# Optimization experiments

Hardware: AMD Instinct MI355X
Metric: run time of the kernel (lower is better)

## Reference

```python
import jax, jax.numpy as jnp
import numpy as np

B, T, E, H = 4, 1024, 1024, 16
D = E // H  # head_size = 64
EPS = 1e-5


def layernorm(x, g, b):
    mu = jnp.mean(x, axis=-1, keepdims=True)
    var = jnp.mean(jnp.square(x - mu), axis=-1, keepdims=True)
    return (x - mu) * jax.lax.rsqrt(var + EPS) * g + b


def setup_inputs() -> dict:
    key = jax.random.key(0)
    ks = jax.random.split(key, 12)
    s = 0.02
    return {
        "x": jax.random.normal(ks[0], (B, T, E), dtype=jnp.float32),
        "ln1_g": jnp.ones((E,), jnp.float32),
        "ln1_b": jnp.zeros((E,), jnp.float32),
        "Wq": jax.random.normal(ks[1], (H, E, D), dtype=jnp.float32) * s,
        "Wk": jax.random.normal(ks[2], (H, E, D), dtype=jnp.float32) * s,
        "Wv": jax.random.normal(ks[3], (H, E, D), dtype=jnp.float32) * s,
        "Wp": jax.random.normal(ks[4], (E, E), dtype=jnp.float32) * s,
        "bp": jnp.zeros((E,), jnp.float32),
        "ln2_g": jnp.ones((E,), jnp.float32),
        "ln2_b": jnp.zeros((E,), jnp.float32),
        "W1": jax.random.normal(ks[5], (E, 4 * E), dtype=jnp.float32) * s,
        "b1": jnp.zeros((4 * E,), jnp.float32),
        "W2": jax.random.normal(ks[6], (4 * E, E), dtype=jnp.float32) * s,
        "b2": jnp.zeros((E,), jnp.float32),
    }


def reference(x, ln1_g, ln1_b, Wq, Wk, Wv, Wp, bp, ln2_g, ln2_b, W1, b1, W2, b2):
    # --- attention sub-block (pre-LN) ---
    h = layernorm(x, ln1_g, ln1_b)               # [B,T,E]
    q = jnp.einsum('bte,hed->bhtd', h, Wq)       # [B,H,T,D]
    k = jnp.einsum('bte,hed->bhtd', h, Wk)
    v = jnp.einsum('bte,hed->bhtd', h, Wv)
    # NOTE: original module has NO 1/sqrt(D) scaling and its 'tril' buffer is
    # all-ones, so masked_fill is a no-op -> full (non-causal) softmax.
    scores = jnp.einsum('bhtd,bhsd->bhts', q, k)  # [B,H,T,T]
    attn = jax.nn.softmax(scores, axis=-1)
    o = jnp.einsum('bhts,bhsd->bhtd', attn, v)    # [B,H,T,D]
    o = o.transpose(0, 2, 1, 3).reshape(x.shape[0], x.shape[1], -1)  # [B,T,E]
    x = x + o @ Wp + bp
    # --- feedforward sub-block (dropout is identity at eval) ---
    h2 = layernorm(x, ln2_g, ln2_b)
    x = x + jax.nn.relu(h2 @ W1 + b1) @ W2 + b2
    return x
```

## Files before the change

### kernel.cpp

```cpp
#include <hip/hip_runtime.h>
#include <hip/hip_bf16.h>

#define BB 4
#define TT 1024
#define EE 1024
#define HH 16
#define DD 64
#define MM 4096
#define NQKV 3072
#define E4 4096

using short8  = __attribute__((ext_vector_type(8))) short;
using short4v = __attribute__((ext_vector_type(4))) short;
using f32x4   = __attribute__((ext_vector_type(4))) float;

__device__ __forceinline__ short f2bf(float f) {
    __hip_bfloat16 h = __float2bfloat16(f);
    return *reinterpret_cast<short*>(&h);
}

__device__ __forceinline__ unsigned int cvtpk_bf16(float a, float b) {
    unsigned int w;
    asm("v_cvt_pk_bf16_f32 %0, %1, %2" : "=v"(w) : "v"(a), "v"(b));
    return w;
}

__device__ __forceinline__ void gld16(const void* g, void* l) {
    __builtin_amdgcn_global_load_lds((__attribute__((address_space(1))) void*)g,
                                     (__attribute__((address_space(3))) void*)l,
                                     16, 0, 0);
}

__global__ __launch_bounds__(256) void tcvt_kernel(const float* __restrict__ in,
                                                   short* __restrict__ out,
                                                   int R, int C) {
    __shared__ short tile[64][65];
    const int c0 = blockIdx.x * 64, r0 = blockIdx.y * 64;
    const int tr = threadIdx.x >> 6;
    const int tc = threadIdx.x & 63;
#pragma unroll
    for (int i = 0; i < 16; ++i) {
        int r = i * 4 + tr;
        tile[tc][r] = f2bf(in[(size_t)(r0 + r) * C + c0 + tc]);
    }
    __syncthreads();
#pragma unroll
    for (int i = 0; i < 16; ++i) {
        int c = i * 4 + tr;
        out[(size_t)(c0 + c) * R + r0 + tc] = tile[c][tc];
    }
}

__global__ __launch_bounds__(256) void pack_qkv_t(const float* __restrict__ Wq,
                                                  const float* __restrict__ Wk,
                                                  const float* __restrict__ Wv,
                                                  short* __restrict__ out) {
    __shared__ short tile[64][65];
    const int m = blockIdx.y;
    const int which = m >> 4, head = m & 15;
    const float* src = ((which == 0) ? Wq : (which == 1) ? Wk : Wv) + (size_t)head * EE * DD;
    const float scale = (which == 1) ? 1.44269504f : 1.0f;
    const int e0 = blockIdx.x * 64;
    const int tr = threadIdx.x >> 6, tc = threadIdx.x & 63;
#pragma unroll
    for (int i = 0; i < 16; ++i) {
        int e = i * 4 + tr;
        tile[tc][e] = f2bf(src[(size_t)(e0 + e) * DD + tc] * scale);
    }
    __syncthreads();
#pragma unroll
    for (int i = 0; i < 16; ++i) {
        int d = i * 4 + tr;
        out[(size_t)(which * 1024 + head * 64 + d) * EE + e0 + tc] = tile[d][tc];
    }
}

__global__ __launch_bounds__(256) void vtr_kernel(const short* __restrict__ qkv,
                                                  short* __restrict__ vT) {
    __shared__ short tile[64][68];
    const int b = blockIdx.z;
    const int t0 = blockIdx.x * 64, c0 = blockIdx.y * 64;
    const int tr = threadIdx.x >> 4;
    const int q4 = (threadIdx.x & 15) * 4;
#pragma unroll
    for (int i = 0; i < 4; ++i) {
        int t = i * 16 + tr;
        short4v v = *(const short4v*)&qkv[((size_t)b * TT + t0 + t) * NQKV + 2048 + c0 + q4];
        *(short4v*)&tile[t][q4] = v;
    }
    __syncthreads();
#pragma unroll
    for (int i = 0; i < 4; ++i) {
        int c = i * 16 + tr;
        short4v v;
        v[0] = tile[q4 + 0][c];
        v[1] = tile[q4 + 1][c];
        v[2] = tile[q4 + 2][c];
        v[3] = tile[q4 + 3][c];
        *(short4v*)&vT[((size_t)b * 1024 + c0 + c) * TT + t0 + q4] = v;
    }
}

__global__ __launch_bounds__(256) void ln_kernel(const float* __restrict__ x,
                                                 const float* __restrict__ g,
                                                 const float* __restrict__ b,
                                                 short* __restrict__ out) {
    __shared__ float red[4];
    const int row = blockIdx.x;
    const int tid = threadIdx.x;
    float4 v = *(const float4*)&x[(size_t)row * EE + tid * 4];
    float s = v.x + v.y + v.z + v.w;
#pragma unroll
    for (int off = 32; off >= 1; off >>= 1) s += __shfl_xor(s, off, 64);
    if ((tid & 63) == 0) red[tid >> 6] = s;
    __syncthreads();
    float mean = (red[0] + red[1] + red[2] + red[3]) * (1.0f / EE);
    __syncthreads();
    float d0 = v.x - mean, d1 = v.y - mean, d2 = v.z - mean, d3 = v.w - mean;
    s = d0 * d0 + d1 * d1 + d2 * d2 + d3 * d3;
#pragma unroll
    for (int off = 32; off >= 1; off >>= 1) s += __shfl_xor(s, off, 64);
    if ((tid & 63) == 0) red[tid >> 6] = s;
    __syncthreads();
    float var = (red[0] + red[1] + red[2] + red[3]) * (1.0f / EE);
    float rstd = rsqrtf(var + 1e-5f);
    int c = tid * 4;
    short4v o;
    o[0] = f2bf(d0 * rstd * g[c + 0] + b[c + 0]);
    o[1] = f2bf(d1 * rstd * g[c + 1] + b[c + 1]);
    o[2] = f2bf(d2 * rstd * g[c + 2] + b[c + 2]);
    o[3] = f2bf(d3 * rstd * g[c + 3] + b[c + 3]);
    *(short4v*)&out[(size_t)row * EE + c] = o;
}

template <int BN, int PIPE, bool HAS_BIAS, bool RELU, bool RESID, bool OUT_BF16>
__global__ __launch_bounds__(256) void gemm_bt(const short* __restrict__ A,
                                               const short* __restrict__ Bt,
                                               const float* __restrict__ bias,
                                               const float* __restrict__ resid,
                                               void* __restrict__ outp,
                                               int M, int N, int K) {
    constexpr int WRC = (BN == 128) ? 2 : 4;
    constexpr int WCC = (BN == 128) ? 2 : 1;
    constexpr int MI = 8 / WRC;
    constexpr int NI = BN / (16 * WCC);
    constexpr int BCH = BN / 32;
    constexpr int ASZ = 128 * 64, BSZ = BN * 64;

    __shared__ __align__(16) short As[(PIPE ? 2 : 1) * ASZ];
    __shared__ __align__(16) short Bs[(PIPE ? 2 : 1) * BSZ];

    const int tid = threadIdx.x;
    const int lane = tid & 63;
    const int wid = tid >> 6;
    const int wr = (WRC == 2) ? (wid >> 1) : wid;
    const int wc = (WCC == 2) ? (wid & 1) : 0;
    const int l15 = lane & 15, lhi = lane >> 4;

    int wg = blockIdx.y * gridDim.x + blockIdx.x;
    const int chunk = (gridDim.x * gridDim.y) >> 3;
    wg = (wg & 7) * chunk + (wg >> 3);
    const int bx = wg % gridDim.x;
    const int by = wg / gridDim.x;
    const int row0 = by * 128, col0 = bx * BN;

    const int srow = tid >> 3;
    const int scol = (((tid & 7) ^ (srow & 7)) << 3);
    const int rsw = l15 & 7;

    const int wrow0 = wr * (16 * MI);
    const int wcol0 = wc * (16 * NI);

    f32x4 acc[MI][NI] = {};

    auto stage = [&](int k0, int bs) {
#pragma unroll
        for (int ch = 0; ch < 4; ++ch)
            gld16(&A[(size_t)(row0 + ch * 32 + srow) * K + k0 + scol],
                  &As[bs * ASZ + ch * 2048 + wid * 512]);
#pragma unroll
        for (int ch = 0; ch < BCH; ++ch)
            gld16(&Bt[(size_t)(col0 + ch * 32 + srow) * K + k0 + scol],
                  &Bs[bs * BSZ + ch * 2048 + wid * 512]);
    };
    auto compute = [&](int bs) {
#pragma unroll
        for (int ks = 0; ks < 2; ++ks) {
            short8 af[MI], bf[NI];
#pragma unroll
            for (int mi = 0; mi < MI; ++mi)
                af[mi] = *(const short8*)&As[bs * ASZ + (wrow0 + mi * 16 + l15) * 64 +
                                             (((ks << 2) + lhi) ^ rsw) * 8];
#pragma unroll
            for (int ni = 0; ni < NI; ++ni)
                bf[ni] = *(const short8*)&Bs[bs * BSZ + (wcol0 + ni * 16 + l15) * 64 +
                                             (((ks << 2) + lhi) ^ rsw) * 8];
#pragma unroll
            for (int mi = 0; mi < MI; ++mi)
#pragma unroll
                for (int ni = 0; ni < NI; ++ni)
                    acc[mi][ni] = __builtin_amdgcn_mfma_f32_16x16x32_bf16(
                        af[mi], bf[ni], acc[mi][ni], 0, 0, 0);
        }
    };

    if (PIPE == 1) {
        const int nt = K >> 6;
        stage(0, 0);
        stage(64, 1);
        int cur = 0;
        for (int t = 0; t < nt; ++t) {
            if (t + 1 < nt) asm volatile("s_waitcnt vmcnt(6)" ::: "memory");
            else            asm volatile("s_waitcnt vmcnt(0)" ::: "memory");
            __builtin_amdgcn_s_barrier();
            __builtin_amdgcn_sched_barrier(0);
            compute(cur);
            __builtin_amdgcn_sched_barrier(0);
            __builtin_amdgcn_s_barrier();
            if (t + 2 < nt) stage((t + 2) << 6, cur);
            cur ^= 1;
        }
    } else {
        for (int k0 = 0; k0 < K; k0 += 64) {
            __syncthreads();
            stage(k0, 0);
            __syncthreads();
            compute(0);
        }
    }

    float* outf = (float*)outp;
    short* outb = (short*)outp;
#pragma unroll
    for (int mi = 0; mi < MI; ++mi)
#pragma unroll
        for (int ni = 0; ni < NI; ++ni)
#pragma unroll
            for (int r = 0; r < 4; ++r) {
                int row = row0 + wrow0 + mi * 16 + lhi * 4 + r;
                int col = col0 + wcol0 + ni * 16 + l15;
                float v = acc[mi][ni][r];
                if (HAS_BIAS) v += bias[col];
                if (RELU) v = fmaxf(v, 0.f);
                if (RESID) v += resid[(size_t)row * N + col];
                if (OUT_BF16) outb[(size_t)row * N + col] = f2bf(v);
                else outf[(size_t)row * N + col] = v;
            }
}

__global__ __launch_bounds__(256) void attn_kernel(const short* __restrict__ qkv,
                                                   const short* __restrict__ vT,
                                                   short* __restrict__ obuf) {
    __shared__ __align__(16) short Ks[2][64 * 64];
    __shared__ __align__(16) short Vs[2][64 * 64];
    __shared__ __align__(16) unsigned int Pl[4][2][16][40];
    const int tid = threadIdx.x;
    const int lane = tid & 63;
    const int wid = tid >> 6;
    const int l15 = lane & 15, lhi = lane >> 4;
    const int lhi4 = lhi * 4;

    const int nb = ((blockIdx.x & 7) << 6) + (blockIdx.x >> 3);
    const int b = nb >> 7;
    const int h = (nb >> 3) & 15;
    const int q0 = (nb & 7) << 7;
    const size_t rbase = (size_t)b * TT;
    const int hq = h * 64;
    const short* vg = vT + ((size_t)b * 1024 + hq) * TT;

    const int srow = tid >> 3;
    const int scol = (((tid & 7) ^ (srow & 7)) << 3);
    const int rsw = (l15 & 7);

    short8 aq[2][2];
#pragma unroll
    for (int g = 0; g < 2; ++g)
#pragma unroll
        for (int ks = 0; ks < 2; ++ks)
            aq[g][ks] = *(const short8*)&qkv[(rbase + q0 + wid * 32 + g * 16 + l15) * NQKV +
                                             hq + ks * 32 + lhi * 8];

    float mrun[2] = {-INFINITY, -INFINITY};
    float lsum[2] = {0.f, 0.f};
    f32x4 o[2][4] = {};

#pragma unroll
    for (int ch = 0; ch < 2; ++ch) {
        gld16(&qkv[(rbase + 0 + ch * 32 + srow) * NQKV + 1024 + hq + scol],
              &Ks[0][ch * 2048 + wid * 512]);
        gld16(&vg[(size_t)(ch * 32 + srow) * TT + 0 + scol],
              &Vs[0][ch * 2048 + wid * 512]);
    }
    __syncthreads();

    int cur = 0;
    for (int st = 0; st < TT; st += 64) {
        if (st + 64 < TT) {
#pragma unroll
            for (int ch = 0; ch < 2; ++ch) {
                gld16(&qkv[(rbase + st + 64 + ch * 32 + srow) * NQKV + 1024 + hq + scol],
                      &Ks[cur ^ 1][ch * 2048 + wid * 512]);
                gld16(&vg[(size_t)(ch * 32 + srow) * TT + st + 64 + scol],
                      &Vs[cur ^ 1][ch * 2048 + wid * 512]);
            }
        }
        const short* K = &Ks[cur][0];
        const short* V = &Vs[cur][0];

        short8 kf[4][2];
#pragma unroll
        for (int nt = 0; nt < 4; ++nt)
#pragma unroll
            for (int ks = 0; ks < 2; ++ks)
                kf[nt][ks] = *(const short8*)&K[(nt * 16 + l15) * 64 +
                                               (((ks << 2) + lhi) ^ rsw) * 8];

        short8 pa[2][2];
#pragma unroll
        for (int g = 0; g < 2; ++g) {
            f32x4 stv[4] = {};
#pragma unroll
            for (int nt = 0; nt < 4; ++nt)
#pragma unroll
                for (int ks = 0; ks < 2; ++ks)
                    stv[nt] = __builtin_amdgcn_mfma_f32_16x16x32_bf16(
                        kf[nt][ks], aq[g][ks], stv[nt], 0, 0, 0);
            float tn[4];
#pragma unroll
            for (int nt = 0; nt < 4; ++nt)
                tn[nt] = fmaxf(fmaxf(stv[nt][0], stv[nt][1]),
                               fmaxf(stv[nt][2], stv[nt][3]));
            float tm = fmaxf(fmaxf(tn[0], tn[1]), fmaxf(tn[2], tn[3]));
            tm = fmaxf(tm, __shfl_xor(tm, 16, 64));
            tm = fmaxf(tm, __shfl_xor(tm, 32, 64));
            const bool full = !__all(tm - mrun[g] <= 11.5f);
            if (full) {
                float mnew = fmaxf(mrun[g], tm);
                float fac = exp2f(mrun[g] - mnew);
                mrun[g] = mnew;
                lsum[g] *= fac;
                float f0 = __shfl(fac, lhi4 + 0, 64);
                float f1 = __shfl(fac, lhi4 + 1, 64);
                float f2 = __shfl(fac, lhi4 + 2, 64);
                float f3 = __shfl(fac, lhi4 + 3, 64);
#pragma unroll
                for (int dt = 0; dt < 4; ++dt) {
                    o[g][dt][0] *= f0; o[g][dt][1] *= f1;
                    o[g][dt][2] *= f2; o[g][dt][3] *= f3;
                }
            }
            float pv[4][4];
            float sn[4];
#pragma unroll
            for (int nt = 0; nt < 4; ++nt) {
#pragma unroll
                for (int r = 0; r < 4; ++r) pv[nt][r] = exp2f(stv[nt][r] - mrun[g]);
                sn[nt] = (pv[nt][0] + pv[nt][1]) + (pv[nt][2] + pv[nt][3]);
            }
            float rs = (sn[0] + sn[1]) + (sn[2] + sn[3]);
            rs += __shfl_xor(rs, 16, 64);
            rs += __shfl_xor(rs, 32, 64);
            lsum[g] += rs;
#pragma unroll
            for (int nt = 0; nt < 4; ++nt) {
                uint2 ww;
                ww.x = cvtpk_bf16(pv[nt][0], pv[nt][1]);
                ww.y = cvtpk_bf16(pv[nt][2], pv[nt][3]);
                *(uint2*)&Pl[wid][g][l15][nt * 8 + lhi * 2] = ww;
            }
            pa[g][0] = *(const short8*)&Pl[wid][g][l15][lhi4];
            pa[g][1] = *(const short8*)&Pl[wid][g][l15][16 + lhi4];
        }

        short8 vf[4][2];
#pragma unroll
        for (int dt = 0; dt < 4; ++dt)
#pragma unroll
            for (int k2 = 0; k2 < 2; ++k2)
                vf[dt][k2] = *(const short8*)&V[(dt * 16 + l15) * 64 +
                                               (((k2 << 2) + lhi) ^ rsw) * 8];
#pragma unroll
        for (int g = 0; g < 2; ++g)
#pragma unroll
            for (int dt = 0; dt < 4; ++dt)
#pragma unroll
                for (int k2 = 0; k2 < 2; ++k2)
                    o[g][dt] = __builtin_amdgcn_mfma_f32_16x16x32_bf16(
                        pa[g][k2], vf[dt][k2], o[g][dt], 0, 0, 0);

        __syncthreads();
        cur ^= 1;
    }
#pragma unroll
    for (int g = 0; g < 2; ++g) {
        float inv = 1.0f / lsum[g];
        float i0 = __shfl(inv, lhi4 + 0, 64);
        float i1 = __shfl(inv, lhi4 + 1, 64);
        float i2 = __shfl(inv, lhi4 + 2, 64);
        float i3 = __shfl(inv, lhi4 + 3, 64);
#pragma unroll
        for (int dt = 0; dt < 4; ++dt) {
            int col = hq + dt * 16 + l15;
            size_t rw = rbase + q0 + wid * 32 + g * 16 + lhi4;
            obuf[(rw + 0) * EE + col] = f2bf(o[g][dt][0] * i0);
            obuf[(rw + 1) * EE + col] = f2bf(o[g][dt][1] * i1);
            obuf[(rw + 2) * EE + col] = f2bf(o[g][dt][2] * i2);
            obuf[(rw + 3) * EE + col] = f2bf(o[g][dt][3] * i3);
        }
    }
}

extern "C" void kernel_launch(void* const* d_in, const int* in_sizes, int n_in,
                              void* d_out, int out_size, void* d_ws, size_t ws_size,
                              hipStream_t stream) {
    const float* x   = (const float*)d_in[0];
    const float* g1  = (const float*)d_in[1];
    const float* be1 = (const float*)d_in[2];
    const float* Wq  = (const float*)d_in[3];
    const float* Wk  = (const float*)d_in[4];
    const float* Wv  = (const float*)d_in[5];
    const float* Wp  = (const float*)d_in[6];
    const float* bp  = (const float*)d_in[7];
    const float* g2  = (const float*)d_in[8];
    const float* be2 = (const float*)d_in[9];
    const float* W1  = (const float*)d_in[10];
    const float* b1f = (const float*)d_in[11];
    const float* W2  = (const float*)d_in[12];
    const float* b2f = (const float*)d_in[13];

    char* p = (char*)d_ws;
    short* h_bf   = (short*)p; p += (size_t)MM * EE * 2;
    short* wqkv   = (short*)p; p += (size_t)EE * NQKV * 2;
    short* qkv    = (short*)p; p += (size_t)MM * NQKV * 2;
    short* o_bf   = (short*)p; p += (size_t)MM * EE * 2;
    short* wp_bf  = (short*)p; p += (size_t)EE * EE * 2;
    float* x1     = (float*)p; p += (size_t)MM * EE * 4;
    short* h2_bf  = (short*)p; p += (size_t)MM * EE * 2;
    short* w1_bf  = (short*)p; p += (size_t)EE * E4 * 2;
    short* mid_bf = (short*)p; p += (size_t)MM * E4 * 2;
    short* w2_bf  = (short*)p; p += (size_t)E4 * EE * 2;
    short* vTb    = (short*)p; p += (size_t)BB * 1024 * TT * 2;

    pack_qkv_t<<<dim3(16, 48), 256, 0, stream>>>(Wq, Wk, Wv, wqkv);
    tcvt_kernel<<<dim3(16, 16), 256, 0, stream>>>(Wp, wp_bf, EE, EE);
    tcvt_kernel<<<dim3(64, 16), 256, 0, stream>>>(W1, w1_bf, EE, E4);
    tcvt_kernel<<<dim3(16, 64), 256, 0, stream>>>(W2, w2_bf, E4, EE);

    ln_kernel<<<MM, 256, 0, stream>>>(x, g1, be1, h_bf);

    gemm_bt<128, 0, false, false, false, true>
        <<<dim3(NQKV / 128, MM / 128), 256, 0, stream>>>(h_bf, wqkv, nullptr, nullptr,
                                                         qkv, MM, NQKV, EE);

    vtr_kernel<<<dim3(16, 16, BB), 256, 0, stream>>>(qkv, vTb);

    attn_kernel<<<BB * HH * (TT / 128), 256, 0, stream>>>(qkv, vTb, o_bf);

    gemm_bt<64, 1, true, false, true, false>
        <<<dim3(EE / 64, MM / 128), 256, 0, stream>>>(o_bf, wp_bf, bp, x, x1, MM, EE, EE);

    ln_kernel<<<MM, 256, 0, stream>>>(x1, g2, be2, h2_bf);

    gemm_bt<128, 0, true, true, false, true>
        <<<dim3(E4 / 128, MM / 128), 256, 0, stream>>>(h2_bf, w1_bf, b1f, nullptr,
                                                       mid_bf, MM, E4, EE);

    gemm_bt<64, 1, true, false, true, false>
        <<<dim3(EE / 64, MM / 128), 256, 0, stream>>>(mid_bf, w2_bf, b2f, x1,
                                                      (float*)d_out, MM, EE, E4);
}
```

Baseline: 235.3 us.

## Add 256x256-tile pipelined GEMM for QKV and FFN1 projections

Adds a new 512-thread GEMM kernel with 256x256 output tiles, XOR-swizzled LDS staging, double-buffered async global-to-LDS loads interleaved with MFMA phases, workgroup remapping across XCDs, and s_setprio around MFMA bursts. It replaces the 128x128 non-pipelined GEMM for the QKV projection and the first FFN layer. Larger tiles raise arithmetic intensity and the pipelining is meant to hide load latency. In exchange the grid gets much smaller (12x16 and 16x16 blocks), which risks underfilling the device's compute units, and register pressure rises from 32 accumulator tiles per thread.

Result: faster. 221.3 us (-5.9%).

```diff
diff --git a/kernel.cpp b/kernel.cpp
--- a/kernel.cpp
+++ b/kernel.cpp
@@ -131,6 +131,119 @@
     o[2] = f2bf(d2 * rstd * g[c + 2] + b[c + 2]);
     o[3] = f2bf(d3 * rstd * g[c + 3] + b[c + 3]);
     *(short4v*)&out[(size_t)row * EE + c] = o;
+}
+
+template <bool HAS_BIAS, bool RELU>
+__global__ __launch_bounds__(512, 2) void gemm256(const short* __restrict__ A,
+                                                  const short* __restrict__ Bt,
+                                                  const float* __restrict__ bias,
+                                                  short* __restrict__ out,
+                                                  int M, int N, int K) {
+    __shared__ __align__(16) short Ab[2][2][8192];
+    __shared__ __align__(16) short Bb[2][2][8192];
+
+    const int tid = threadIdx.x;
+    const int lane = tid & 63;
+    const int wid = tid >> 6;
+    const int wr = wid >> 2;
+    const int wc = wid & 3;
+    const int l15 = lane & 15, lhi = lane >> 4;
+    const int rsw = l15 & 7;
+
+    int wg = blockIdx.y * gridDim.x + blockIdx.x;
+    const int chunk = (gridDim.x * gridDim.y) >> 3;
+    wg = (wg & 7) * chunk + (wg >> 3);
+    const int bx = wg % gridDim.x, by = wg / gridDim.x;
+    const int row0 = by * 256, col0 = bx * 256;
+
+    const int srow = tid >> 3;
+    const int scol = (((tid & 7) ^ (srow & 7)) << 3);
+
+    const int NT = K >> 6;
+
+    f32x4 acc[8][4] = {};
+
+    auto stageA = [&](int b, int h, int k0) {
+#pragma unroll
+        for (int j = 0; j < 2; ++j)
+            gld16(&A[(size_t)(row0 + h * 128 + j * 64 + srow) * K + k0 + scol],
+                  &Ab[b][h][j * 4096 + wid * 512]);
+    };
+    auto stageB = [&](int b, int h, int k0) {
+#pragma unroll
+        for (int j = 0; j < 2; ++j)
+            gld16(&Bt[(size_t)(col0 + h * 128 + j * 64 + srow) * K + k0 + scol],
+                  &Bb[b][h][j * 4096 + wid * 512]);
+    };
+
+    stageA(0, 0, 0); stageA(0, 1, 0);
+    stageB(0, 0, 0); stageB(0, 1, 0);
+    if (NT > 1) {
+        stageB(1, 0, 64); stageB(1, 1, 64);
+        asm volatile("s_waitcnt vmcnt(4)" ::: "memory");
+    } else {
+        asm volatile("s_waitcnt vmcnt(0)" ::: "memory");
+    }
+    __builtin_amdgcn_s_barrier();
+
+    for (int u = 0; u < NT; ++u) {
+        const int buf = u & 1;
+        short8 bfr[4][2];
+#pragma unroll
+        for (int p = 0; p < 4; ++p) {
+            if (p == 0) {
+#pragma unroll
+                for (int n = 0; n < 4; ++n)
+#pragma unroll
+                    for (int ks = 0; ks < 2; ++ks)
+                        bfr[n][ks] = *(const short8*)&Bb[buf][wc >> 1]
+                            [((wc & 1) * 64 + n * 16 + l15) * 64 +
+                             (((ks << 2) + lhi) ^ rsw) * 8];
+            }
+            short8 af[2][2];
+#pragma unroll
+            for (int mi = 0; mi < 2; ++mi)
+#pragma unroll
+                for (int ks = 0; ks < 2; ++ks)
+                    af[mi][ks] = *(const short8*)&Ab[buf][wr]
+                        [((p * 2 + mi) * 16 + l15) * 64 +
+                         (((ks << 2) + lhi) ^ rsw) * 8];
+            if (p == 0 && u + 1 < NT) stageA(buf ^ 1, 0, (u + 1) << 6);
+            if (p == 1 && u + 1 < NT) stageA(buf ^ 1, 1, (u + 1) << 6);
+            if (p == 2 && u + 2 < NT) stageB(buf, 0, (u + 2) << 6);
+            if (p == 3 && u + 2 < NT) stageB(buf, 1, (u + 2) << 6);
+            __builtin_amdgcn_s_barrier();
+            __builtin_amdgcn_s_setprio(1);
+#pragma unroll
+            for (int mi = 0; mi < 2; ++mi)
+#pragma unroll
+                for (int n = 0; n < 4; ++n)
+#pragma unroll
+                    for (int ks = 0; ks < 2; ++ks)
+                        acc[p * 2 + mi][n] = __builtin_amdgcn_mfma_f32_16x16x32_bf16(
+                            af[mi][ks], bfr[n][ks], acc[p * 2 + mi][n], 0, 0, 0);
+            __builtin_amdgcn_s_setprio(0);
+            if (p == 3 && u + 1 < NT) {
+                if (u + 2 < NT) asm volatile("s_waitcnt vmcnt(4)" ::: "memory");
+                else            asm volatile("s_waitcnt vmcnt(0)" ::: "memory");
+            }
+            __builtin_amdgcn_s_barrier();
+        }
+    }
+
+#pragma unroll
+    for (int m = 0; m < 8; ++m)
+#pragma unroll
+        for (int n = 0; n < 4; ++n)
+#pragma unroll
+            for (int r = 0; r < 4; ++r) {
+                int row = row0 + wr * 128 + m * 16 + lhi * 4 + r;
+                int col = col0 + wc * 64 + n * 16 + l15;
+                float v = acc[m][n][r];
+                if (HAS_BIAS) v += bias[col];
+                if (RELU) v = fmaxf(v, 0.f);
+                out[(size_t)row * N + col] = f2bf(v);
+            }
 }
 
 template <int BN, int PIPE, bool HAS_BIAS, bool RELU, bool RESID, bool OUT_BF16>
@@ -448,8 +561,8 @@
 
     ln_kernel<<<MM, 256, 0, stream>>>(x, g1, be1, h_bf);
 
-    gemm_bt<128, 0, false, false, false, true>
-        <<<dim3(NQKV / 128, MM / 128), 256, 0, stream>>>(h_bf, wqkv, nullptr, nullptr,
+    gemm256<false, false>
+        <<<dim3(NQKV / 256, MM / 256), 512, 0, stream>>>(h_bf, wqkv, nullptr,
                                                          qkv, MM, NQKV, EE);
 
     vtr_kernel<<<dim3(16, 16, BB), 256, 0, stream>>>(qkv, vTb);
@@ -461,8 +574,8 @@
 
     ln_kernel<<<MM, 256, 0, stream>>>(x1, g2, be2, h2_bf);
 
-    gemm_bt<128, 0, true, true, false, true>
-        <<<dim3(E4 / 128, MM / 128), 256, 0, stream>>>(h2_bf, w1_bf, b1f, nullptr,
+    gemm256<true, true>
+        <<<dim3(E4 / 256, MM / 256), 512, 0, stream>>>(h2_bf, w1_bf, b1f,
                                                        mid_bf, MM, E4, EE);
 
     gemm_bt<64, 1, true, false, true, false>
```
